# Kernel optimization log

Hardware: AMD Instinct MI355X
Metric: run time of the kernel (lower is better)

Reference implementation:

```python
import jax, jax.numpy as jnp
import numpy as np

BN_EPS = 1e-5


def setup_inputs() -> dict:
    key = jax.random.key(0)
    ks = jax.random.split(key, 6)
    B, S, M, D = 4096, 50, 20, 512
    return {
        "image_feats": jax.random.normal(ks[0], (B, S, D), dtype=jnp.float32),
        "text_feats": jax.random.normal(ks[1], (M, 2, D), dtype=jnp.float32),
        "rad_feat": jax.random.randint(ks[2], (B, M), 0, 2, dtype=jnp.int32),
        "valid_mask": jax.random.randint(ks[3], (B, S), 0, 2, dtype=jnp.int32),
        "bn_gamma": jnp.ones((2 * D,), dtype=jnp.float32),
        "bn_beta": jnp.zeros((2 * D,), dtype=jnp.float32),
        "bn_mean": jax.random.normal(ks[4], (2 * D,), dtype=jnp.float32),
        "bn_var": jax.random.uniform(ks[5], (2 * D,), dtype=jnp.float32, minval=0.5, maxval=1.5),
        "w_cls": jax.random.normal(ks[5], (2, 2 * D), dtype=jnp.float32) * 0.02,
        "b_cls": jnp.zeros((2,), dtype=jnp.float32),
    }


def _l2norm(x):
    return x / jnp.linalg.norm(x, axis=-1, keepdims=True)


def reference(image_feats, text_feats, rad_feat, valid_mask, bn_gamma, bn_beta, bn_mean, bn_var, w_cls, b_cls):
    B, S, D = image_feats.shape
    M = text_feats.shape[0]
    # ragged gather: text_feats[j][rad_feat[i, j]] -> [B, M, D]
    text_latents = _l2norm(text_feats[jnp.arange(M)[None, :], rad_feat])
    # per-frame image latents, L2-normalized then masked (padding-to-max_len equivalent)
    mask = (valid_mask == 1).astype(image_feats.dtype)  # [B, S]
    img = _l2norm(image_feats) * mask[..., None]        # [B, S, D]
    # attention pooling over ragged valid frames
    aw = jnp.einsum("bmd,bsd->bms", text_latents, img)  # [B, M, S]
    attn_image = aw.mean(axis=1)                          # [B, S] (mean over M)
    cnt = jnp.maximum(mask.sum(axis=1, keepdims=True), 1.0)
    attn_text = aw.sum(axis=2) / cnt                      # [B, M] (mean over valid frames)
    img_pool = _l2norm(jnp.einsum("bs,bsd->bd", attn_image, img))
    txt_pool = _l2norm(jnp.einsum("bm,bmd->bd", attn_text, text_latents))
    combined = jnp.concatenate([img_pool, txt_pool], axis=1)  # [B, 2D]
    # fusion: ReLU -> Dropout(eval=identity) -> BatchNorm1d(eval, running stats)
    h = jax.nn.relu(combined)
    h = (h - bn_mean) * jax.lax.rsqrt(bn_var + BN_EPS) * bn_gamma + bn_beta
    return h @ w_cls.T + b_cls
```

## Files before the change

### kernel.cpp

```cpp
#include <hip/hip_runtime.h>
#include <math.h>

#define D_ 512
#define S_ 50
#define M_ 20
#define BN_EPS_ 1e-5f

template <int CTRL, int RM>
__device__ __forceinline__ float dpp_step(float x) {
    int t = __builtin_amdgcn_update_dpp(0, __float_as_int(x), CTRL, RM, 0xf, true);
    return x + __int_as_float(t);
}
__device__ __forceinline__ float wave_sum(float x) {
    x = dpp_step<0x111, 0xf>(x);
    x = dpp_step<0x112, 0xf>(x);
    x = dpp_step<0x114, 0xf>(x);
    x = dpp_step<0x118, 0xf>(x);
    x = dpp_step<0x142, 0xa>(x);
    x = dpp_step<0x143, 0xc>(x);
    return __int_as_float(__builtin_amdgcn_readlane(__float_as_int(x), 63));
}

__global__ __launch_bounds__(512) void setup_kernel(
    const float* __restrict__ tf, const float* __restrict__ gamma,
    const float* __restrict__ beta, const float* __restrict__ mean,
    const float* __restrict__ var, const float* __restrict__ wcls,
    const float* __restrict__ bcls, float* __restrict__ ws)
{
    float* tnorm = ws;
    float* wf    = ws + 2 * M_ * D_;
    float* bf    = wf + 4 * D_;
    const int tid  = threadIdx.x;
    const int lane = tid & 63;
    const int wv   = tid >> 6;

    if (blockIdx.x < 5) {
        const int row = blockIdx.x * 8 + wv;
        const float4* p = (const float4*)(tf + (size_t)row * D_) + lane * 2;
        float4 a = p[0], b = p[1];
        float ss = a.x*a.x + a.y*a.y + a.z*a.z + a.w*a.w
                 + b.x*b.x + b.y*b.y + b.z*b.z + b.w*b.w;
        ss = wave_sum(ss);
        float inv = rsqrtf(ss);
        float4 na = {a.x*inv, a.y*inv, a.z*inv, a.w*inv};
        float4 nb = {b.x*inv, b.y*inv, b.z*inv, b.w*inv};
        float4* q = (float4*)(tnorm + (size_t)row * D_) + lane * 2;
        q[0] = na; q[1] = nb;
    } else {
        __shared__ float r0[8], r1[8];
        float pa = 0.f, pb = 0.f;
        for (int c = tid; c < 2 * D_; c += 512) {
            float s1 = rsqrtf(var[c] + BN_EPS_) * gamma[c];
            float w0 = wcls[c], w1 = wcls[2 * D_ + c];
            wf[c] = w0 * s1;
            wf[2 * D_ + c] = w1 * s1;
            float bmc = beta[c] - mean[c] * s1;
            pa += bmc * w0;
            pb += bmc * w1;
        }
        pa = wave_sum(pa);
        pb = wave_sum(pb);
        if (lane == 0) { r0[wv] = pa; r1[wv] = pb; }
        __syncthreads();
        if (tid == 0) {
            float A = 0.f, Bv = 0.f;
            #pragma unroll
            for (int w = 0; w < 8; ++w) { A += r0[w]; Bv += r1[w]; }
            bf[0] = bcls[0] + A;
            bf[1] = bcls[1] + Bv;
        }
    }
}

__global__ __launch_bounds__(256, 5) void main_kernel(
    const float* __restrict__ img, const int* __restrict__ rad,
    const int* __restrict__ vm, const float* __restrict__ ws,
    float* __restrict__ out)
{
    const float* tnorm = ws;
    const float* wf    = ws + 2 * M_ * D_;
    const float* bf    = wf + 4 * D_;
    const int tid  = threadIdx.x;
    const int lane = tid & 63;
    const int wv   = tid >> 6;
    const int b    = blockIdx.x;

    __shared__ float shTA[4][D_];
    __shared__ float accS[4][D_];
    __shared__ float accP[4][D_];

    int vmv  = (lane < S_) ? vm[(size_t)b * S_ + lane] : 0;
    int radv = (lane < M_) ? rad[(size_t)b * M_ + lane] : 0;
    unsigned long long bal = __ballot(lane < S_ && vmv == 1);
    float cnt_inv = 1.0f / fmaxf((float)__popcll(bal), 1.0f);

    unsigned long long wb = bal & (0x1111111111111111ULL << wv);
    const float* imgb = img + (size_t)b * S_ * D_;

    int sA = -1, sB = -1, sC = -1;
    float4 A0{}, A1{}, B0{}, B1{}, C0{}, C1{};
    if (wb) {
        sA = __ffsll(wb) - 1; wb &= wb - 1;
        const float4* p = (const float4*)(imgb + (size_t)sA * D_) + lane * 2;
        A0 = p[0]; A1 = p[1];
    }
    if (wb) {
        sB = __ffsll(wb) - 1; wb &= wb - 1;
        const float4* p = (const float4*)(imgb + (size_t)sB * D_) + lane * 2;
        B0 = p[0]; B1 = p[1];
    }
    if (wb) {
        sC = __ffsll(wb) - 1; wb &= wb - 1;
        const float4* p = (const float4*)(imgb + (size_t)sC * D_) + lane * 2;
        C0 = p[0]; C1 = p[1];
    }

    float tbp[8] = {0,0,0,0,0,0,0,0};
    #pragma unroll
    for (int k = 0; k < M_ / 4; ++k) {
        int m  = wv + 4 * k;
        int rm = __builtin_amdgcn_readlane(radv, m);
        const float4* p = (const float4*)(tnorm + (size_t)(2 * m + rm) * D_) + lane * 2;
        float4 x = p[0], y = p[1];
        tbp[0] += x.x; tbp[1] += x.y; tbp[2] += x.z; tbp[3] += x.w;
        tbp[4] += y.x; tbp[5] += y.y; tbp[6] += y.z; tbp[7] += y.w;
    }
    #pragma unroll
    for (int j = 0; j < 8; ++j) shTA[wv][j * 64 + lane] = tbp[j];
    __syncthreads();

    float tb[8];
    #pragma unroll
    for (int j = 0; j < 8; ++j) {
        float s = shTA[0][j * 64 + lane] + shTA[1][j * 64 + lane]
                + shTA[2][j * 64 + lane] + shTA[3][j * 64 + lane];
        tb[j] = s * (1.0f / (float)M_);
    }

    float isum[8]  = {0,0,0,0,0,0,0,0};
    float ipool[8] = {0,0,0,0,0,0,0,0};
    while (sA >= 0) {
        float v[8] = {A0.x, A0.y, A0.z, A0.w, A1.x, A1.y, A1.z, A1.w};
        float ss = 0.f, ar = 0.f;
        #pragma unroll
        for (int j = 0; j < 8; ++j) { ss += v[j] * v[j]; ar += tb[j] * v[j]; }
        ss = wave_sum(ss);
        ar = wave_sum(ar);
        float inv = rsqrtf(ss);
        float w2  = ar * inv * inv;
        #pragma unroll
        for (int j = 0; j < 8; ++j) {
            isum[j]  += v[j] * inv;
            ipool[j] += v[j] * w2;
        }
        sA = sB; A0 = B0; A1 = B1;
        sB = sC; B0 = C0; B1 = C1;
        sC = -1;
        if (wb) {
            sC = __ffsll(wb) - 1; wb &= wb - 1;
            const float4* p = (const float4*)(imgb + (size_t)sC * D_) + lane * 2;
            C0 = p[0]; C1 = p[1];
        }
    }
    #pragma unroll
    for (int j = 0; j < 8; ++j) {
        accS[wv][j * 64 + lane] = isum[j];
        accP[wv][j * 64 + lane] = ipool[j];
    }
    __syncthreads();

    float as8[8];
    #pragma unroll
    for (int j = 0; j < 8; ++j)
        as8[j] = accS[0][j * 64 + lane] + accS[1][j * 64 + lane]
               + accS[2][j * 64 + lane] + accS[3][j * 64 + lane];

    float tpp[8] = {0,0,0,0,0,0,0,0};
    #pragma unroll
    for (int k = 0; k < M_ / 4; ++k) {
        int m  = wv + 4 * k;
        int rm = __builtin_amdgcn_readlane(radv, m);
        const float4* p = (const float4*)(tnorm + (size_t)(2 * m + rm) * D_) + lane * 2;
        float4 x = p[0], y = p[1];
        float tv[8] = {x.x, x.y, x.z, x.w, y.x, y.y, y.z, y.w};
        float d = 0.f;
        #pragma unroll
        for (int j = 0; j < 8; ++j) d += tv[j] * as8[j];
        float a = wave_sum(d) * cnt_inv;
        #pragma unroll
        for (int j = 0; j < 8; ++j) tpp[j] += a * tv[j];
    }
    #pragma unroll
    for (int j = 0; j < 8; ++j) shTA[wv][j * 64 + lane] = tpp[j];
    __syncthreads();

    if (wv != 0) return;

    const float4* w00 = (const float4*)(wf)          + lane * 2;
    const float4* w01 = (const float4*)(wf + D_)     + lane * 2;
    const float4* w10 = (const float4*)(wf + 2 * D_) + lane * 2;
    const float4* w11 = (const float4*)(wf + 3 * D_) + lane * 2;
    float4 a0 = w00[0], a1 = w00[1], b0 = w01[0], b1 = w01[1];
    float4 c0 = w10[0], c1 = w10[1], d0 = w11[0], d1 = w11[1];

    float ap8[8], tp8[8];
    float ipl = 0.f, tpl = 0.f;
    #pragma unroll
    for (int j = 0; j < 8; ++j) {
        ap8[j] = accP[0][j * 64 + lane] + accP[1][j * 64 + lane]
               + accP[2][j * 64 + lane] + accP[3][j * 64 + lane];
        tp8[j] = shTA[0][j * 64 + lane] + shTA[1][j * 64 + lane]
               + shTA[2][j * 64 + lane] + shTA[3][j * 64 + lane];
        ipl += ap8[j] * ap8[j];
        tpl += tp8[j] * tp8[j];
    }
    float inv_ip = rsqrtf(wave_sum(ipl));
    float inv_tp = rsqrtf(wave_sum(tpl));

    float wA[8] = {a0.x,a0.y,a0.z,a0.w,a1.x,a1.y,a1.z,a1.w};
    float wB[8] = {b0.x,b0.y,b0.z,b0.w,b1.x,b1.y,b1.z,b1.w};
    float wC[8] = {c0.x,c0.y,c0.z,c0.w,c1.x,c1.y,c1.z,c1.w};
    float wD[8] = {d0.x,d0.y,d0.z,d0.w,d1.x,d1.y,d1.z,d1.w};
    float o0 = 0.f, o1 = 0.f;
    #pragma unroll
    for (int j = 0; j < 8; ++j) {
        float h1 = fmaxf(ap8[j] * inv_ip, 0.f);
        float h2 = fmaxf(tp8[j] * inv_tp, 0.f);
        o0 += h1 * wA[j] + h2 * wB[j];
        o1 += h1 * wC[j] + h2 * wD[j];
    }
    o0 = wave_sum(o0);
    o1 = wave_sum(o1);
    if (lane == 0) {
        float2 r = {o0 + bf[0], o1 + bf[1]};
        *(float2*)(out + (size_t)b * 2) = r;
    }
}

extern "C" void kernel_launch(void* const* d_in, const int* in_sizes, int n_in,
                              void* d_out, int out_size, void* d_ws, size_t ws_size,
                              hipStream_t stream) {
    const float* img   = (const float*)d_in[0];
    const float* tf    = (const float*)d_in[1];
    const int*   rad   = (const int*)d_in[2];
    const int*   vmsk  = (const int*)d_in[3];
    const float* gamma = (const float*)d_in[4];
    const float* beta  = (const float*)d_in[5];
    const float* mean  = (const float*)d_in[6];
    const float* var   = (const float*)d_in[7];
    const float* wcls  = (const float*)d_in[8];
    const float* bcls  = (const float*)d_in[9];
    float* out = (float*)d_out;
    float* ws  = (float*)d_ws;

    const int B = in_sizes[0] / (S_ * D_);

    setup_kernel<<<6, 512, 0, stream>>>(tf, gamma, beta, mean, var, wcls, bcls, ws);
    main_kernel<<<B, 256, 0, stream>>>(img, rad, vmsk, ws, out);
}
```

Baseline: 49.37 us.

## Fold setup kernel into main kernel, normalizing text rows and BN inline

Removes the separate setup kernel that pre-normalized the text features and folded BatchNorm into the classifier weights. Each block now L2-normalizes its gathered text rows on the fly, keeping per-row inverse norms in registers for the second pass, and applies BatchNorm directly before the classifier dot product. This drops one kernel launch and the dependency between the two kernels, at the cost of redundant per-block normalization math, extra wave reductions, and more parameter loads and registers in the final wave.

```diff
diff --git a/kernel.cpp b/kernel.cpp
--- a/kernel.cpp
+++ b/kernel.cpp
@@ -21,65 +21,14 @@
     return __int_as_float(__builtin_amdgcn_readlane(__float_as_int(x), 63));
 }
 
-__global__ __launch_bounds__(512) void setup_kernel(
-    const float* __restrict__ tf, const float* __restrict__ gamma,
-    const float* __restrict__ beta, const float* __restrict__ mean,
-    const float* __restrict__ var, const float* __restrict__ wcls,
-    const float* __restrict__ bcls, float* __restrict__ ws)
-{
-    float* tnorm = ws;
-    float* wf    = ws + 2 * M_ * D_;
-    float* bf    = wf + 4 * D_;
-    const int tid  = threadIdx.x;
-    const int lane = tid & 63;
-    const int wv   = tid >> 6;
-
-    if (blockIdx.x < 5) {
-        const int row = blockIdx.x * 8 + wv;
-        const float4* p = (const float4*)(tf + (size_t)row * D_) + lane * 2;
-        float4 a = p[0], b = p[1];
-        float ss = a.x*a.x + a.y*a.y + a.z*a.z + a.w*a.w
-                 + b.x*b.x + b.y*b.y + b.z*b.z + b.w*b.w;
-        ss = wave_sum(ss);
-        float inv = rsqrtf(ss);
-        float4 na = {a.x*inv, a.y*inv, a.z*inv, a.w*inv};
-        float4 nb = {b.x*inv, b.y*inv, b.z*inv, b.w*inv};
-        float4* q = (float4*)(tnorm + (size_t)row * D_) + lane * 2;
-        q[0] = na; q[1] = nb;
-    } else {
-        __shared__ float r0[8], r1[8];
-        float pa = 0.f, pb = 0.f;
-        for (int c = tid; c < 2 * D_; c += 512) {
-            float s1 = rsqrtf(var[c] + BN_EPS_) * gamma[c];
-            float w0 = wcls[c], w1 = wcls[2 * D_ + c];
-            wf[c] = w0 * s1;
-            wf[2 * D_ + c] = w1 * s1;
-            float bmc = beta[c] - mean[c] * s1;
-            pa += bmc * w0;
-            pb += bmc * w1;
-        }
-        pa = wave_sum(pa);
-        pb = wave_sum(pb);
-        if (lane == 0) { r0[wv] = pa; r1[wv] = pb; }
-        __syncthreads();
-        if (tid == 0) {
-            float A = 0.f, Bv = 0.f;
-            #pragma unroll
-            for (int w = 0; w < 8; ++w) { A += r0[w]; Bv += r1[w]; }
-            bf[0] = bcls[0] + A;
-            bf[1] = bcls[1] + Bv;
-        }
-    }
-}
-
 __global__ __launch_bounds__(256, 5) void main_kernel(
-    const float* __restrict__ img, const int* __restrict__ rad,
-    const int* __restrict__ vm, const float* __restrict__ ws,
+    const float* __restrict__ img, const float* __restrict__ tf,
+    const int* __restrict__ rad, const int* __restrict__ vm,
+    const float* __restrict__ gamma, const float* __restrict__ beta,
+    const float* __restrict__ mean, const float* __restrict__ var,
+    const float* __restrict__ wcls, const float* __restrict__ bcls,
     float* __restrict__ out)
 {
-    const float* tnorm = ws;
-    const float* wf    = ws + 2 * M_ * D_;
-    const float* bf    = wf + 4 * D_;
     const int tid  = threadIdx.x;
     const int lane = tid & 63;
     const int wv   = tid >> 6;
@@ -115,15 +64,22 @@
         C0 = p[0]; C1 = p[1];
     }
 
+    float inv_m[5];
     float tbp[8] = {0,0,0,0,0,0,0,0};
     #pragma unroll
     for (int k = 0; k < M_ / 4; ++k) {
         int m  = wv + 4 * k;
         int rm = __builtin_amdgcn_readlane(radv, m);
-        const float4* p = (const float4*)(tnorm + (size_t)(2 * m + rm) * D_) + lane * 2;
+        const float4* p = (const float4*)(tf + (size_t)(2 * m + rm) * D_) + lane * 2;
         float4 x = p[0], y = p[1];
-        tbp[0] += x.x; tbp[1] += x.y; tbp[2] += x.z; tbp[3] += x.w;
-        tbp[4] += y.x; tbp[5] += y.y; tbp[6] += y.z; tbp[7] += y.w;
+        float tv[8] = {x.x, x.y, x.z, x.w, y.x, y.y, y.z, y.w};
+        float ss = 0.f;
+        #pragma unroll
+        for (int j = 0; j < 8; ++j) ss += tv[j] * tv[j];
+        float inv = rsqrtf(wave_sum(ss));
+        inv_m[k] = inv;
+        #pragma unroll
+        for (int j = 0; j < 8; ++j) tbp[j] += tv[j] * inv;
     }
     #pragma unroll
     for (int j = 0; j < 8; ++j) shTA[wv][j * 64 + lane] = tbp[j];
@@ -180,9 +136,11 @@
     for (int k = 0; k < M_ / 4; ++k) {
         int m  = wv + 4 * k;
         int rm = __builtin_amdgcn_readlane(radv, m);
-        const float4* p = (const float4*)(tnorm + (size_t)(2 * m + rm) * D_) + lane * 2;
+        const float4* p = (const float4*)(tf + (size_t)(2 * m + rm) * D_) + lane * 2;
         float4 x = p[0], y = p[1];
-        float tv[8] = {x.x, x.y, x.z, x.w, y.x, y.y, y.z, y.w};
+        float inv = inv_m[k];
+        float tv[8] = {x.x * inv, x.y * inv, x.z * inv, x.w * inv,
+                       y.x * inv, y.y * inv, y.z * inv, y.w * inv};
         float d = 0.f;
         #pragma unroll
         for (int j = 0; j < 8; ++j) d += tv[j] * as8[j];
@@ -196,12 +154,18 @@
 
     if (wv != 0) return;
 
-    const float4* w00 = (const float4*)(wf)          + lane * 2;
-    const float4* w01 = (const float4*)(wf + D_)     + lane * 2;
-    const float4* w10 = (const float4*)(wf + 2 * D_) + lane * 2;
-    const float4* w11 = (const float4*)(wf + 3 * D_) + lane * 2;
-    float4 a0 = w00[0], a1 = w00[1], b0 = w01[0], b1 = w01[1];
-    float4 c0 = w10[0], c1 = w10[1], d0 = w11[0], d1 = w11[1];
+    const int o = lane * 2;
+    const float4* g4 = (const float4*)gamma;
+    const float4* b4 = (const float4*)beta;
+    const float4* m4 = (const float4*)mean;
+    const float4* v4 = (const float4*)var;
+    const float4* w4 = (const float4*)wcls;
+    float4 g0a = g4[o], g0b = g4[o + 1], g1a = g4[o + 128], g1b = g4[o + 129];
+    float4 be0a = b4[o], be0b = b4[o + 1], be1a = b4[o + 128], be1b = b4[o + 129];
+    float4 mn0a = m4[o], mn0b = m4[o + 1], mn1a = m4[o + 128], mn1b = m4[o + 129];
+    float4 vr0a = v4[o], vr0b = v4[o + 1], vr1a = v4[o + 128], vr1b = v4[o + 129];
+    float4 w00a = w4[o], w00b = w4[o + 1], w01a = w4[o + 128], w01b = w4[o + 129];
+    float4 w10a = w4[o + 256], w10b = w4[o + 257], w11a = w4[o + 384], w11b = w4[o + 385];
 
     float ap8[8], tp8[8];
     float ipl = 0.f, tpl = 0.f;
@@ -217,22 +181,33 @@
     float inv_ip = rsqrtf(wave_sum(ipl));
     float inv_tp = rsqrtf(wave_sum(tpl));
 
-    float wA[8] = {a0.x,a0.y,a0.z,a0.w,a1.x,a1.y,a1.z,a1.w};
-    float wB[8] = {b0.x,b0.y,b0.z,b0.w,b1.x,b1.y,b1.z,b1.w};
-    float wC[8] = {c0.x,c0.y,c0.z,c0.w,c1.x,c1.y,c1.z,c1.w};
-    float wD[8] = {d0.x,d0.y,d0.z,d0.w,d1.x,d1.y,d1.z,d1.w};
+    float gI[8] = {g0a.x,g0a.y,g0a.z,g0a.w,g0b.x,g0b.y,g0b.z,g0b.w};
+    float gT[8] = {g1a.x,g1a.y,g1a.z,g1a.w,g1b.x,g1b.y,g1b.z,g1b.w};
+    float bI[8] = {be0a.x,be0a.y,be0a.z,be0a.w,be0b.x,be0b.y,be0b.z,be0b.w};
+    float bT[8] = {be1a.x,be1a.y,be1a.z,be1a.w,be1b.x,be1b.y,be1b.z,be1b.w};
+    float mI[8] = {mn0a.x,mn0a.y,mn0a.z,mn0a.w,mn0b.x,mn0b.y,mn0b.z,mn0b.w};
+    float mT[8] = {mn1a.x,mn1a.y,mn1a.z,mn1a.w,mn1b.x,mn1b.y,mn1b.z,mn1b.w};
+    float vI[8] = {vr0a.x,vr0a.y,vr0a.z,vr0a.w,vr0b.x,vr0b.y,vr0b.z,vr0b.w};
+    float vT[8] = {vr1a.x,vr1a.y,vr1a.z,vr1a.w,vr1b.x,vr1b.y,vr1b.z,vr1b.w};
+    float wA[8] = {w00a.x,w00a.y,w00a.z,w00a.w,w00b.x,w00b.y,w00b.z,w00b.w};
+    float wB[8] = {w01a.x,w01a.y,w01a.z,w01a.w,w01b.x,w01b.y,w01b.z,w01b.w};
+    float wC[8] = {w10a.x,w10a.y,w10a.z,w10a.w,w10b.x,w10b.y,w10b.z,w10b.w};
+    float wD[8] = {w11a.x,w11a.y,w11a.z,w11a.w,w11b.x,w11b.y,w11b.z,w11b.w};
+
     float o0 = 0.f, o1 = 0.f;
     #pragma unroll
     for (int j = 0; j < 8; ++j) {
         float h1 = fmaxf(ap8[j] * inv_ip, 0.f);
+        h1 = (h1 - mI[j]) * rsqrtf(vI[j] + BN_EPS_) * gI[j] + bI[j];
         float h2 = fmaxf(tp8[j] * inv_tp, 0.f);
+        h2 = (h2 - mT[j]) * rsqrtf(vT[j] + BN_EPS_) * gT[j] + bT[j];
         o0 += h1 * wA[j] + h2 * wB[j];
         o1 += h1 * wC[j] + h2 * wD[j];
     }
     o0 = wave_sum(o0);
     o1 = wave_sum(o1);
     if (lane == 0) {
-        float2 r = {o0 + bf[0], o1 + bf[1]};
+        float2 r = {o0 + bcls[0], o1 + bcls[1]};
         *(float2*)(out + (size_t)b * 2) = r;
     }
 }
@@ -251,10 +226,9 @@
     const float* wcls  = (const float*)d_in[8];
     const float* bcls  = (const float*)d_in[9];
     float* out = (float*)d_out;
-    float* ws  = (float*)d_ws;
 
     const int B = in_sizes[0] / (S_ * D_);
 
-    setup_kernel<<<6, 512, 0, stream>>>(tf, gamma, beta, mean, var, wcls, bcls, ws);
-    main_kernel<<<B, 256, 0, stream>>>(img, rad, vmsk, ws, out);
-}
+    main_kernel<<<B, 256, 0, stream>>>(img, tf, rad, vmsk, gamma, beta, mean, var,
+                                       wcls, bcls, out);
+}
```

After: 56.00 us. 13.4% more time.
